# Kernel optimization log

Measured on AMD Instinct MI355X. Metric: run time of the kernel, lower is better.

Reference implementation:

```python
import jax, jax.numpy as jnp
import numpy as np

LN_EPS = 1e-5
GATE_EPS = 1e-9
TOP_K = 2
CAP_FACTOR = 1.0


def reference(x, gamma, beta, wg, W1, b1, W2, b2):
    B, S, H = x.shape
    E = wg.shape[1]
    T = B * S
    K = TOP_K
    C = int(np.ceil(K * T / E * CAP_FACTOR))  # per-expert capacity

    xf = x.reshape(T, H)
    # LayerNorm
    mu = jnp.mean(xf, axis=-1, keepdims=True)
    var = jnp.mean(jnp.square(xf - mu), axis=-1, keepdims=True)
    xn = (xf - mu) * jax.lax.rsqrt(var + LN_EPS) * gamma + beta

    # Gating (DeepSpeed top-k gate, softmax over experts)
    logits = xn @ wg                       # [T,E]
    gates = jax.nn.softmax(logits, axis=-1)
    vals, idx = jax.lax.top_k(gates, K)    # [T,K]

    # Capacity-aware positions: slot j priorities come after slots <j counts
    counts = jnp.zeros((E,), jnp.int32)
    pos_l, keep_l = [], []
    for j in range(K):
        oh = jax.nn.one_hot(idx[:, j], E, dtype=jnp.int32)  # [T,E]
        loc = jnp.cumsum(oh, axis=0) - 1 + counts[None, :]
        pos = jnp.sum(loc * oh, axis=1)                      # [T]
        counts = counts + jnp.sum(oh, axis=0)
        pos_l.append(pos)
        keep_l.append(pos < C)
    pos_k = jnp.stack(pos_l, axis=1)                         # [T,K]
    keep_k = jnp.stack(keep_l, axis=1)                       # [T,K]

    # Normalize kept gate values (DeepSpeed normalizes after capacity drop)
    kept = vals * keep_k.astype(vals.dtype)
    w = kept / (jnp.sum(kept, axis=1, keepdims=True) + GATE_EPS)  # [T,K]

    # Load-balancing aux loss (top-1 assignment counts, DeepSpeed style)
    me = jnp.mean(gates, axis=0)
    ce = jnp.mean(jax.nn.one_hot(idx[:, 0], E, dtype=gates.dtype), axis=0)
    l_aux = jnp.mean(me * ce) * E * E

    # Dispatch: scatter tokens into [E, C+1, H]; dropped tokens go to slot C (discarded)
    buf = jnp.zeros((E, C + 1, H), xn.dtype)
    pos_pad = jnp.where(keep_k, pos_k, C)                    # [T,K]
    for j in range(K):
        buf = buf.at[idx[:, j], pos_pad[:, j]].add(xn)

    # Grouped expert MLP
    h1 = jax.nn.gelu(jnp.einsum('ech,ehf->ecf', buf, W1) + b1[:, None, :], approximate=False)
    y = jnp.einsum('ecf,efh->ech', h1, W2) + b2[:, None, :]   # [E,C+1,H]

    # Combine: gather each token's expert outputs, weight, sum
    outf = jnp.zeros((T, H), x.dtype)
    for j in range(K):
        outf = outf + w[:, j, None] * y[idx[:, j], pos_pad[:, j]]

    out = x + outf.reshape(B, S, H)
    return out, l_aux, counts.astype(jnp.float32)


def setup_inputs() -> dict:
    key = jax.random.key(0)
    ks = jax.random.split(key, 6)
    H, E, F = 1024, 8, 4096
    x = jax.random.normal(ks[0], (2, 2048, H), jnp.float32)
    return {
        'x': x,
        'gamma': jnp.ones((H,), jnp.float32),
        'beta': jnp.zeros((H,), jnp.float32),
        'wg': jax.random.normal(ks[1], (H, E), jnp.float32) * 0.02,
        'W1': jax.random.normal(ks[2], (E, H, F), jnp.float32) * 0.02,
        'b1': jnp.zeros((E, F), jnp.float32),
        'W2': jax.random.normal(ks[3], (E, F, H), jnp.float32) * 0.02,
        'b2': jnp.zeros((E, H), jnp.float32),
    }
```

## Files before the change

kernel.cpp:

```cpp
#include <hip/hip_runtime.h>
#include <hip/hip_bf16.h>
#include <math.h>


#define T_TOK 4096
#define HD 1024
#define NE 8
#define FD 4096
#define CAPN 1024

typedef __attribute__((ext_vector_type(8))) short short8;
typedef __attribute__((ext_vector_type(4))) float f32x4;

__device__ __forceinline__ unsigned short f2b(float f) {
  __hip_bfloat16 h = __float2bfloat16(f);
  unsigned short u;
  __builtin_memcpy(&u, &h, 2);
  return u;
}

__global__ __launch_bounds__(256) void k_ln_gate(
    const float* __restrict__ x, const float* __restrict__ gamma,
    const float* __restrict__ beta, const float* __restrict__ wg,
    unsigned short* __restrict__ xn, float* __restrict__ gates,
    float2* __restrict__ vals, int2* __restrict__ eidx) {
  const int t = blockIdx.x;
  const int tid = threadIdx.x;
  const int lane = tid & 63, wid = tid >> 6;
  __shared__ float red[4];
  __shared__ float pr[4][8];

  const float4 v = ((const float4*)(x + (size_t)t * HD))[tid];
  float s = v.x + v.y + v.z + v.w;
#pragma unroll
  for (int o = 32; o > 0; o >>= 1) s += __shfl_down(s, o);
  if (lane == 0) red[wid] = s;
  __syncthreads();
  const float mean = (red[0] + red[1] + red[2] + red[3]) * (1.0f / HD);
  float dv[4];
  dv[0] = v.x - mean; dv[1] = v.y - mean; dv[2] = v.z - mean; dv[3] = v.w - mean;
  float q = dv[0]*dv[0] + dv[1]*dv[1] + dv[2]*dv[2] + dv[3]*dv[3];
  __syncthreads();
#pragma unroll
  for (int o = 32; o > 0; o >>= 1) q += __shfl_down(q, o);
  if (lane == 0) red[wid] = q;
  __syncthreads();
  const float var = (red[0] + red[1] + red[2] + red[3]) * (1.0f / HD);
  const float rs = 1.0f / sqrtf(var + 1e-5f);

  const float4 gm = ((const float4*)gamma)[tid];
  const float4 bt = ((const float4*)beta)[tid];
  float xv[4];
  xv[0] = dv[0] * rs * gm.x + bt.x;
  xv[1] = dv[1] * rs * gm.y + bt.y;
  xv[2] = dv[2] * rs * gm.z + bt.z;
  xv[3] = dv[3] * rs * gm.w + bt.w;
  ushort4 o4;
  o4.x = f2b(xv[0]); o4.y = f2b(xv[1]); o4.z = f2b(xv[2]); o4.w = f2b(xv[3]);
  ((ushort4*)(xn + (size_t)t * HD))[tid] = o4;

  float p[8];
#pragma unroll
  for (int e = 0; e < 8; e++) p[e] = 0.f;
  const int c0 = tid * 4;
#pragma unroll
  for (int i = 0; i < 4; i++) {
    const float4 w0 = ((const float4*)(wg + (size_t)(c0 + i) * NE))[0];
    const float4 w1 = ((const float4*)(wg + (size_t)(c0 + i) * NE))[1];
    p[0] += xv[i] * w0.x; p[1] += xv[i] * w0.y;
    p[2] += xv[i] * w0.z; p[3] += xv[i] * w0.w;
    p[4] += xv[i] * w1.x; p[5] += xv[i] * w1.y;
    p[6] += xv[i] * w1.z; p[7] += xv[i] * w1.w;
  }
#pragma unroll
  for (int e = 0; e < 8; e++)
#pragma unroll
    for (int o = 32; o > 0; o >>= 1) p[e] += __shfl_down(p[e], o);
  if (lane == 0) {
#pragma unroll
    for (int e = 0; e < 8; e++) pr[wid][e] = p[e];
  }
  __syncthreads();
  if (tid == 0) {
    float lg[8];
#pragma unroll
    for (int e = 0; e < 8; e++) lg[e] = pr[0][e] + pr[1][e] + pr[2][e] + pr[3][e];
    float mx = lg[0];
#pragma unroll
    for (int e = 1; e < 8; e++) mx = fmaxf(mx, lg[e]);
    float ex[8], sum = 0.f;
#pragma unroll
    for (int e = 0; e < 8; e++) { ex[e] = expf(lg[e] - mx); sum += ex[e]; }
    const float inv = 1.0f / sum;
    float g[8];
#pragma unroll
    for (int e = 0; e < 8; e++) { g[e] = ex[e] * inv; gates[(size_t)t * 8 + e] = g[e]; }
    int i0 = 0;
    for (int e = 1; e < 8; e++) if (g[e] > g[i0]) i0 = e;
    int i1 = (i0 == 0) ? 1 : 0;
    for (int e = 0; e < 8; e++) if (e != i0 && g[e] > g[i1]) i1 = e;
    vals[t] = make_float2(g[i0], g[i1]);
    eidx[t] = make_int2(i0, i1);
  }
}

__global__ __launch_bounds__(64) void k_scan(
    const int2* __restrict__ eidx, const float2* __restrict__ vals,
    const float* __restrict__ gates, int* __restrict__ ppad,
    float2* __restrict__ w, float* __restrict__ out_tail) {
  __shared__ int s0[T_TOK], s1[T_TOK];
  const int lane = threadIdx.x;
  for (int i = lane; i < T_TOK; i += 64) {
    int2 e2 = eidx[i];
    s0[i] = e2.x; s1[i] = e2.y;
  }
  __syncthreads();
  const unsigned long long lt = (lane == 63) ? 0x7fffffffffffffffull
                                             : ((1ull << lane) - 1ull);
  int cnt[8], ce[8];
#pragma unroll
  for (int e = 0; e < 8; e++) cnt[e] = 0;
  for (int j = 0; j < 2; j++) {
    const int* sj = j ? s1 : s0;
    for (int base = 0; base < T_TOK; base += 64) {
      const int my = sj[base + lane];
      int pos = 0;
#pragma unroll
      for (int e = 0; e < 8; e++) {
        unsigned long long m = __ballot(my == e);
        if (my == e) pos = cnt[e] + __popcll(m & lt);
        cnt[e] += __popcll(m);
      }
      ppad[(base + lane) * 2 + j] = (pos < CAPN) ? pos : CAPN;
    }
    if (j == 0) {
#pragma unroll
      for (int e = 0; e < 8; e++) ce[e] = cnt[e];
    }
  }
  for (int base = 0; base < T_TOK; base += 64) {
    const int t = base + lane;
    const float2 v = vals[t];
    const int p0 = ppad[2 * t], p1 = ppad[2 * t + 1];
    const float k0 = (p0 < CAPN) ? v.x : 0.f;
    const float k1 = (p1 < CAPN) ? v.y : 0.f;
    const float inv = 1.0f / (k0 + k1 + 1e-9f);
    w[t] = make_float2(k0 * inv, k1 * inv);
  }
  float acc[8];
#pragma unroll
  for (int e = 0; e < 8; e++) acc[e] = 0.f;
  for (int t = lane; t < T_TOK; t += 64) {
    const float4 a = ((const float4*)(gates + (size_t)t * 8))[0];
    const float4 b = ((const float4*)(gates + (size_t)t * 8))[1];
    acc[0] += a.x; acc[1] += a.y; acc[2] += a.z; acc[3] += a.w;
    acc[4] += b.x; acc[5] += b.y; acc[6] += b.z; acc[7] += b.w;
  }
#pragma unroll
  for (int e = 0; e < 8; e++)
#pragma unroll
    for (int o = 32; o > 0; o >>= 1) acc[e] += __shfl_down(acc[e], o);
  if (lane == 0) {
    float la = 0.f;
#pragma unroll
    for (int e = 0; e < 8; e++)
      la += (acc[e] * (1.0f / T_TOK)) * ((float)ce[e] * (1.0f / T_TOK));
    out_tail[0] = la * 8.0f;
#pragma unroll
    for (int e = 0; e < 8; e++) out_tail[1 + e] = (float)cnt[e];
  }
}

__global__ __launch_bounds__(128) void k_scatter(
    const unsigned short* __restrict__ xn, const int2* __restrict__ eidx,
    const int* __restrict__ ppad, unsigned short* __restrict__ buf) {
  const int b = blockIdx.x;
  const int t = b >> 1, j = b & 1;
  const int pp = ppad[2 * t + j];
  if (pp >= CAPN) return;
  const int2 e2 = eidx[t];
  const int e = j ? e2.y : e2.x;
  const uint4* s = (const uint4*)(xn + (size_t)t * HD);
  uint4* d = (uint4*)(buf + ((size_t)e * CAPN + pp) * HD);
  d[threadIdx.x] = s[threadIdx.x];
}

__global__ __launch_bounds__(256) void k_convT(
    const float* __restrict__ Win, unsigned short* __restrict__ Wout,
    int R, int C) {
  __shared__ __align__(16) unsigned short tile[64][72];
  const int e = blockIdx.z;
  const int c0 = blockIdx.x * 64, r0 = blockIdx.y * 64;
  const int tid = threadIdx.x;
  const int r = tid >> 2, qq = tid & 3;
  const float* src = Win + ((size_t)e * R + r0 + r) * C + c0;
#pragma unroll
  for (int i = 0; i < 4; i++) {
    const int cc = qq * 16 + i * 4;
    const float4 v = *(const float4*)(src + cc);
    tile[cc + 0][r] = f2b(v.x);
    tile[cc + 1][r] = f2b(v.y);
    tile[cc + 2][r] = f2b(v.z);
    tile[cc + 3][r] = f2b(v.w);
  }
  __syncthreads();
  const int cr = tid >> 2;
  unsigned short* dst = Wout + ((size_t)e * C + c0 + cr) * R + r0 + qq * 16;
  *(uint4*)(dst + 0) = *(const uint4*)&tile[cr][qq * 16];
  *(uint4*)(dst + 8) = *(const uint4*)&tile[cr][qq * 16 + 8];
}

template <int MODE>
__global__ __launch_bounds__(256) void k_gemm(
    const unsigned short* __restrict__ A, const unsigned short* __restrict__ Bt,
    const float* __restrict__ bias, void* __restrict__ out) {
  constexpr int K = MODE ? FD : HD;
  constexpr int N = MODE ? HD : FD;
  const int nt = blockIdx.x, mt = blockIdx.y;
  const int e = mt >> 3;
  const size_t m0 = (size_t)mt * 128;
  const int n0 = nt * 128;
  __shared__ __align__(16) unsigned short lA[128 * 32];
  __shared__ __align__(16) unsigned short lB[128 * 32];
  const int tid = threadIdx.x;
  const int lane = tid & 63, wid = tid >> 6;
  const int sr = tid >> 2, sq = tid & 3;
  const unsigned short* gA = A + m0 * (size_t)K + (size_t)sq * 8;
  const unsigned short* gB = Bt + ((size_t)e * N + n0) * K + (size_t)sq * 8;
  const int wr = wid >> 1, wc = wid & 1;
  const int l15 = lane & 15, half = lane >> 4;

  f32x4 acc[4][4];
  const f32x4 fz = {0.f, 0.f, 0.f, 0.f};
#pragma unroll
  for (int mi = 0; mi < 4; mi++)
#pragma unroll
    for (int ni = 0; ni < 4; ni++) acc[mi][ni] = fz;

  for (int k0 = 0; k0 < K; k0 += 32) {
    __syncthreads();
    __builtin_amdgcn_global_load_lds(
        (const __attribute__((address_space(1))) void*)(gA + (size_t)sr * K + k0),
        (__attribute__((address_space(3))) void*)(lA + wid * 512), 16, 0, 0);
    __builtin_amdgcn_global_load_lds(
        (const __attribute__((address_space(1))) void*)(gA + (size_t)(sr + 64) * K + k0),
        (__attribute__((address_space(3))) void*)(lA + 2048 + wid * 512), 16, 0, 0);
    __builtin_amdgcn_global_load_lds(
        (const __attribute__((address_space(1))) void*)(gB + (size_t)sr * K + k0),
        (__attribute__((address_space(3))) void*)(lB + wid * 512), 16, 0, 0);
    __builtin_amdgcn_global_load_lds(
        (const __attribute__((address_space(1))) void*)(gB + (size_t)(sr + 64) * K + k0),
        (__attribute__((address_space(3))) void*)(lB + 2048 + wid * 512), 16, 0, 0);
    __syncthreads();
    short8 af[4], bfr[4];
#pragma unroll
    for (int i = 0; i < 4; i++) {
      af[i]  = *(const short8*)&lA[(wr * 64 + i * 16 + l15) * 32 + half * 8];
      bfr[i] = *(const short8*)&lB[(wc * 64 + i * 16 + l15) * 32 + half * 8];
    }
#pragma unroll
    for (int mi = 0; mi < 4; mi++)
#pragma unroll
      for (int ni = 0; ni < 4; ni++)
        acc[mi][ni] = __builtin_amdgcn_mfma_f32_16x16x32_bf16(af[mi], bfr[ni],
                                                              acc[mi][ni], 0, 0, 0);
  }

  const float* brow = bias + (size_t)e * N;
  if (MODE == 0) {
    unsigned short* h1 = (unsigned short*)out;
#pragma unroll
    for (int mi = 0; mi < 4; mi++)
#pragma unroll
      for (int ni = 0; ni < 4; ni++) {
        const int col = n0 + wc * 64 + ni * 16 + l15;
        const float bv = brow[col];
#pragma unroll
        for (int r = 0; r < 4; r++) {
          const size_t row = m0 + wr * 64 + mi * 16 + half * 4 + r;
          const float pre = acc[mi][ni][r] + bv;
          const float g = 0.5f * pre * (1.0f + erff(pre * 0.70710678118654752f));
          h1[row * (size_t)N + col] = f2b(g);
        }
      }
  } else {
    float* y = (float*)out;
#pragma unroll
    for (int mi = 0; mi < 4; mi++)
#pragma unroll
      for (int ni = 0; ni < 4; ni++) {
        const int col = n0 + wc * 64 + ni * 16 + l15;
        const float bv = brow[col];
#pragma unroll
        for (int r = 0; r < 4; r++) {
          const size_t row = m0 + wr * 64 + mi * 16 + half * 4 + r;
          y[row * (size_t)N + col] = acc[mi][ni][r] + bv;
        }
      }
  }
}

__global__ __launch_bounds__(256) void k_combine(
    const float* __restrict__ x, const float* __restrict__ y,
    const int2* __restrict__ eidx, const int* __restrict__ ppad,
    const float2* __restrict__ w, float* __restrict__ out) {
  const int t = blockIdx.x, tid = threadIdx.x;
  const float2 wt = w[t];
  const int2 e2 = eidx[t];
  const int p0 = ppad[2 * t], p1 = ppad[2 * t + 1];
  float4 o = ((const float4*)(x + (size_t)t * HD))[tid];
  if (p0 < CAPN) {
    const float4 a = ((const float4*)(y + ((size_t)e2.x * CAPN + p0) * HD))[tid];
    o.x += wt.x * a.x; o.y += wt.x * a.y; o.z += wt.x * a.z; o.w += wt.x * a.w;
  }
  if (p1 < CAPN) {
    const float4 a = ((const float4*)(y + ((size_t)e2.y * CAPN + p1) * HD))[tid];
    o.x += wt.y * a.x; o.y += wt.y * a.y; o.z += wt.y * a.z; o.w += wt.y * a.w;
  }
  ((float4*)(out + (size_t)t * HD))[tid] = o;
}

extern "C" void kernel_launch(void* const* d_in, const int* in_sizes, int n_in,
                              void* d_out, int out_size, void* d_ws, size_t ws_size,
                              hipStream_t stream) {
  const float* x     = (const float*)d_in[0];
  const float* gamma = (const float*)d_in[1];
  const float* beta  = (const float*)d_in[2];
  const float* wg    = (const float*)d_in[3];
  const float* W1    = (const float*)d_in[4];
  const float* b1    = (const float*)d_in[5];
  const float* W2    = (const float*)d_in[6];
  const float* b2    = (const float*)d_in[7];
  float* out = (float*)d_out;

  char* ws = (char*)d_ws;
  unsigned short* xn  = (unsigned short*)(ws);
  unsigned short* buf = (unsigned short*)(ws + (8ull << 20));
  unsigned short* h1  = (unsigned short*)(ws + (24ull << 20));
  float* y            = (float*)(ws + (88ull << 20));
  unsigned short* WT  = (unsigned short*)(ws + (120ull << 20));
  float* gates        = (float*)(ws + (184ull << 20));
  float2* vals        = (float2*)(ws + (184ull << 20) + (128ull << 10));
  int2* eidx          = (int2*)(ws + (184ull << 20) + (160ull << 10));
  int* ppad           = (int*)(ws + (184ull << 20) + (192ull << 10));
  float2* wnrm        = (float2*)(ws + (184ull << 20) + (224ull << 10));

  hipMemsetAsync(buf, 0, (16ull << 20), stream);
  k_ln_gate<<<T_TOK, 256, 0, stream>>>(x, gamma, beta, wg, xn, gates, vals, eidx);
  k_scan<<<1, 64, 0, stream>>>(eidx, vals, gates, ppad, wnrm,
                               out + (size_t)T_TOK * HD);
  k_scatter<<<T_TOK * 2, 128, 0, stream>>>(xn, eidx, ppad, buf);
  k_convT<<<dim3(FD / 64, HD / 64, NE), 256, 0, stream>>>(W1, WT, HD, FD);
  k_gemm<0><<<dim3(FD / 128, 64), 256, 0, stream>>>(buf, WT, b1, h1);
  k_convT<<<dim3(HD / 64, FD / 64, NE), 256, 0, stream>>>(W2, WT, FD, HD);
  k_gemm<1><<<dim3(HD / 128, 64), 256, 0, stream>>>(h1, WT, b2, y);
  k_combine<<<T_TOK, 256, 0, stream>>>(x, y, eidx, ppad, wnrm, out);
}
```

Measured before the change: 633.1 us.

## Use 256x256 pipelined MFMA GEMM with split-K down-projection and fused combine

Replaces the 128x128 single-buffered expert GEMM with a 512-thread, 256x256-tile kernel. It uses a 4-stage LDS ring fed by global_load_lds, XOR-swizzled LDS addressing, explicit waitcnt/barrier scheduling, setprio around the MFMA bursts and a grouped block-index swizzle. The down-projection can split K in two into separate partial buffers, and the combine kernel sums them, adds b2 and computes the capacity-normalized gate weights inline. The buffer memset is dropped and the scan kernel runs the gate-mean reduction on extra waves. The aim is more data reuse per tile and better overlap of loads with MFMA, at the cost of 128KB of LDS per block (one block per CU) and extra fp32 partial-output traffic in the split-K path.

```diff
diff --git a/kernel.cpp b/kernel.cpp
--- a/kernel.cpp
+++ b/kernel.cpp
@@ -104,70 +104,77 @@
   }
 }
 
-__global__ __launch_bounds__(64) void k_scan(
-    const int2* __restrict__ eidx, const float2* __restrict__ vals,
-    const float* __restrict__ gates, int* __restrict__ ppad,
-    float2* __restrict__ w, float* __restrict__ out_tail) {
+__global__ __launch_bounds__(256) void k_scan(
+    const int2* __restrict__ eidx, const float* __restrict__ gates,
+    int* __restrict__ ppad, float* __restrict__ out_tail) {
   __shared__ int s0[T_TOK], s1[T_TOK];
-  const int lane = threadIdx.x;
-  for (int i = lane; i < T_TOK; i += 64) {
+  __shared__ float mw[3][8];
+  __shared__ int ce_sh[8], cnt_sh[8];
+  const int tid = threadIdx.x;
+  const int lane = tid & 63, wid = tid >> 6;
+  for (int i = tid; i < T_TOK; i += 256) {
     int2 e2 = eidx[i];
     s0[i] = e2.x; s1[i] = e2.y;
   }
   __syncthreads();
-  const unsigned long long lt = (lane == 63) ? 0x7fffffffffffffffull
-                                             : ((1ull << lane) - 1ull);
-  int cnt[8], ce[8];
-#pragma unroll
-  for (int e = 0; e < 8; e++) cnt[e] = 0;
-  for (int j = 0; j < 2; j++) {
-    const int* sj = j ? s1 : s0;
-    for (int base = 0; base < T_TOK; base += 64) {
-      const int my = sj[base + lane];
-      int pos = 0;
-#pragma unroll
-      for (int e = 0; e < 8; e++) {
-        unsigned long long m = __ballot(my == e);
-        if (my == e) pos = cnt[e] + __popcll(m & lt);
-        cnt[e] += __popcll(m);
+  if (wid == 0) {
+    const unsigned long long lt = (lane == 63) ? 0x7fffffffffffffffull
+                                               : ((1ull << lane) - 1ull);
+    int cnt[8];
+#pragma unroll
+    for (int e = 0; e < 8; e++) cnt[e] = 0;
+    for (int j = 0; j < 2; j++) {
+      const int* sj = j ? s1 : s0;
+      for (int base = 0; base < T_TOK; base += 64) {
+        const int my = sj[base + lane];
+        int pos = 0;
+#pragma unroll
+        for (int e = 0; e < 8; e++) {
+          unsigned long long m = __ballot(my == e);
+          if (my == e) pos = cnt[e] + __popcll(m & lt);
+          cnt[e] += __popcll(m);
+        }
+        ppad[(base + lane) * 2 + j] = (pos < CAPN) ? pos : CAPN;
       }
-      ppad[(base + lane) * 2 + j] = (pos < CAPN) ? pos : CAPN;
-    }
-    if (j == 0) {
-#pragma unroll
-      for (int e = 0; e < 8; e++) ce[e] = cnt[e];
-    }
-  }
-  for (int base = 0; base < T_TOK; base += 64) {
-    const int t = base + lane;
-    const float2 v = vals[t];
-    const int p0 = ppad[2 * t], p1 = ppad[2 * t + 1];
-    const float k0 = (p0 < CAPN) ? v.x : 0.f;
-    const float k1 = (p1 < CAPN) ? v.y : 0.f;
-    const float inv = 1.0f / (k0 + k1 + 1e-9f);
-    w[t] = make_float2(k0 * inv, k1 * inv);
-  }
-  float acc[8];
-#pragma unroll
-  for (int e = 0; e < 8; e++) acc[e] = 0.f;
-  for (int t = lane; t < T_TOK; t += 64) {
-    const float4 a = ((const float4*)(gates + (size_t)t * 8))[0];
-    const float4 b = ((const float4*)(gates + (size_t)t * 8))[1];
-    acc[0] += a.x; acc[1] += a.y; acc[2] += a.z; acc[3] += a.w;
-    acc[4] += b.x; acc[5] += b.y; acc[6] += b.z; acc[7] += b.w;
-  }
-#pragma unroll
-  for (int e = 0; e < 8; e++)
-#pragma unroll
-    for (int o = 32; o > 0; o >>= 1) acc[e] += __shfl_down(acc[e], o);
-  if (lane == 0) {
+      if (j == 0 && lane == 0) {
+#pragma unroll
+        for (int e = 0; e < 8; e++) ce_sh[e] = cnt[e];
+      }
+    }
+    if (lane == 0) {
+#pragma unroll
+      for (int e = 0; e < 8; e++) cnt_sh[e] = cnt[e];
+    }
+  } else {
+    float acc[8];
+#pragma unroll
+    for (int e = 0; e < 8; e++) acc[e] = 0.f;
+    for (int t = tid - 64; t < T_TOK; t += 192) {
+      const float4 a = ((const float4*)(gates + (size_t)t * 8))[0];
+      const float4 b = ((const float4*)(gates + (size_t)t * 8))[1];
+      acc[0] += a.x; acc[1] += a.y; acc[2] += a.z; acc[3] += a.w;
+      acc[4] += b.x; acc[5] += b.y; acc[6] += b.z; acc[7] += b.w;
+    }
+#pragma unroll
+    for (int e = 0; e < 8; e++)
+#pragma unroll
+      for (int o = 32; o > 0; o >>= 1) acc[e] += __shfl_down(acc[e], o);
+    if (lane == 0) {
+#pragma unroll
+      for (int e = 0; e < 8; e++) mw[wid - 1][e] = acc[e];
+    }
+  }
+  __syncthreads();
+  if (tid == 0) {
     float la = 0.f;
 #pragma unroll
-    for (int e = 0; e < 8; e++)
-      la += (acc[e] * (1.0f / T_TOK)) * ((float)ce[e] * (1.0f / T_TOK));
+    for (int e = 0; e < 8; e++) {
+      const float me = (mw[0][e] + mw[1][e] + mw[2][e]) * (1.0f / T_TOK);
+      la += me * ((float)ce_sh[e] * (1.0f / T_TOK));
+    }
     out_tail[0] = la * 8.0f;
 #pragma unroll
-    for (int e = 0; e < 8; e++) out_tail[1 + e] = (float)cnt[e];
+    for (int e = 0; e < 8; e++) out_tail[1 + e] = (float)cnt_sh[e];
   }
 }
 
@@ -210,112 +217,180 @@
   *(uint4*)(dst + 8) = *(const uint4*)&tile[cr][qq * 16 + 8];
 }
 
-template <int MODE>
-__global__ __launch_bounds__(256) void k_gemm(
+#define GLL16(SRC, DSTOFF) __builtin_amdgcn_global_load_lds( \
+    (const __attribute__((address_space(1))) void*)(SRC), \
+    (__attribute__((address_space(3))) void*)(smem + (DSTOFF)), 16, 0, 0)
+
+#define STAGE_A(T) { const size_t ko = (size_t)(T) * 32; const int rbo = ((T)&3)*32768; \
+  GLL16(gA + ko + oA0, rbo + ldsAd); \
+  GLL16(gA + ko + oA1, rbo + 8192 + ldsAd); }
+
+#define STAGE_B(T) { const size_t ko = (size_t)(T) * 32; const int rbo = ((T)&3)*32768; \
+  GLL16(gB + ko + oA0, rbo + ldsBd); \
+  GLL16(gB + ko + oA1, rbo + 8192 + ldsBd); }
+
+#define TILE(T, DOST, VMW) { \
+  const unsigned char* rb = smem + ((T)&3)*32768; \
+  short8 af[4], bfv[4]; \
+  _Pragma("unroll") for (int i = 0; i < 4; ++i) { \
+    af[i]  = *(const short8*)(rb + offA + i*1024); \
+    bfv[i] = *(const short8*)(rb + offB + i*1024); } \
+  if (DOST) { STAGE_A((T)+3); } \
+  asm volatile("s_barrier" ::: "memory"); \
+  __builtin_amdgcn_s_setprio(1); \
+  _Pragma("unroll") for (int mi = 0; mi < 4; ++mi) \
+    _Pragma("unroll") for (int ni = 0; ni < 4; ++ni) \
+      acc[mi][ni] = __builtin_amdgcn_mfma_f32_16x16x32_bf16(af[mi], bfv[ni], acc[mi][ni], 0, 0, 0); \
+  __builtin_amdgcn_s_setprio(0); \
+  _Pragma("unroll") for (int i = 0; i < 4; ++i) \
+    af[i] = *(const short8*)(rb + offA + 4096 + i*1024); \
+  if (DOST) { STAGE_B((T)+3); } \
+  asm volatile("s_waitcnt lgkmcnt(0)" ::: "memory"); \
+  asm volatile("s_waitcnt vmcnt(" #VMW ")" ::: "memory"); \
+  asm volatile("s_barrier" ::: "memory"); \
+  __builtin_amdgcn_s_setprio(1); \
+  _Pragma("unroll") for (int mi = 0; mi < 4; ++mi) \
+    _Pragma("unroll") for (int ni = 0; ni < 4; ++ni) \
+      acc[4+mi][ni] = __builtin_amdgcn_mfma_f32_16x16x32_bf16(af[mi], bfv[ni], acc[4+mi][ni], 0, 0, 0); \
+  __builtin_amdgcn_s_setprio(0); \
+}
+
+template <int MODE, int SPLITK>
+__global__ __launch_bounds__(512, 2) void k_gemm256(
     const unsigned short* __restrict__ A, const unsigned short* __restrict__ Bt,
     const float* __restrict__ bias, void* __restrict__ out) {
   constexpr int K = MODE ? FD : HD;
   constexpr int N = MODE ? HD : FD;
-  const int nt = blockIdx.x, mt = blockIdx.y;
-  const int e = mt >> 3;
-  const size_t m0 = (size_t)mt * 128;
-  const int n0 = nt * 128;
-  __shared__ __align__(16) unsigned short lA[128 * 32];
-  __shared__ __align__(16) unsigned short lB[128 * 32];
+  constexpr int KLOC = K / SPLITK;
+  constexpr int NT = KLOC / 32;
+  constexpr int NBT = N / 256;
+
+  __shared__ __align__(16) unsigned char smem[4 * 32768];
+
   const int tid = threadIdx.x;
   const int lane = tid & 63, wid = tid >> 6;
-  const int sr = tid >> 2, sq = tid & 3;
-  const unsigned short* gA = A + m0 * (size_t)K + (size_t)sq * 8;
-  const unsigned short* gB = Bt + ((size_t)e * N + n0) * K + (size_t)sq * 8;
-  const int wr = wid >> 1, wc = wid & 1;
-  const int l15 = lane & 15, half = lane >> 4;
-
-  f32x4 acc[4][4];
+  const int l15 = lane & 15, lq = lane >> 4;
+  const int wr = wid >> 2, wc = wid & 3;
+
+  const int nwg = gridDim.x;
+  const int per = nwg >> 3;
+  const int lin = blockIdx.x;
+  const int swz = (lin & 7) * per + (lin >> 3);
+  const int mt = swz & 31;
+  const int rest = swz >> 5;
+  const int nt = rest % NBT;
+  const int z = rest / NBT;
+
+  const int e = mt >> 2;
+  const size_t m0 = (size_t)mt * 256;
+  const int n0 = nt * 256;
+  const unsigned short* gA = A + m0 * (size_t)K + (size_t)z * KLOC;
+  const unsigned short* gB = Bt + ((size_t)e * N + n0) * (size_t)K + (size_t)z * KLOC;
+
+  const int LA0 = tid * 16, LA1 = 8192 + tid * 16;
+  const int r0s = LA0 >> 6, c0s = (LA0 >> 4) & 3;
+  const int r1s = LA1 >> 6, c1s = (LA1 >> 4) & 3;
+  const size_t oA0 = (size_t)r0s * K + (size_t)(c0s ^ ((r0s >> 1) & 3)) * 8;
+  const size_t oA1 = (size_t)r1s * K + (size_t)(c1s ^ ((r1s >> 1) & 3)) * 8;
+  const int ldsAd = wid * 1024;
+  const int ldsBd = 16384 + wid * 1024;
+
+  const int rA = wr * 128 + l15;
+  const int offA = rA * 64 + ((lq ^ ((rA >> 1) & 3)) << 4);
+  const int rB = wc * 64 + l15;
+  const int offB = 16384 + rB * 64 + ((lq ^ ((rB >> 1) & 3)) << 4);
+
+  f32x4 acc[8][4];
   const f32x4 fz = {0.f, 0.f, 0.f, 0.f};
 #pragma unroll
-  for (int mi = 0; mi < 4; mi++)
+  for (int mi = 0; mi < 8; mi++)
 #pragma unroll
     for (int ni = 0; ni < 4; ni++) acc[mi][ni] = fz;
 
-  for (int k0 = 0; k0 < K; k0 += 32) {
-    __syncthreads();
-    __builtin_amdgcn_global_load_lds(
-        (const __attribute__((address_space(1))) void*)(gA + (size_t)sr * K + k0),
-        (__attribute__((address_space(3))) void*)(lA + wid * 512), 16, 0, 0);
-    __builtin_amdgcn_global_load_lds(
-        (const __attribute__((address_space(1))) void*)(gA + (size_t)(sr + 64) * K + k0),
-        (__attribute__((address_space(3))) void*)(lA + 2048 + wid * 512), 16, 0, 0);
-    __builtin_amdgcn_global_load_lds(
-        (const __attribute__((address_space(1))) void*)(gB + (size_t)sr * K + k0),
-        (__attribute__((address_space(3))) void*)(lB + wid * 512), 16, 0, 0);
-    __builtin_amdgcn_global_load_lds(
-        (const __attribute__((address_space(1))) void*)(gB + (size_t)(sr + 64) * K + k0),
-        (__attribute__((address_space(3))) void*)(lB + 2048 + wid * 512), 16, 0, 0);
-    __syncthreads();
-    short8 af[4], bfr[4];
-#pragma unroll
-    for (int i = 0; i < 4; i++) {
-      af[i]  = *(const short8*)&lA[(wr * 64 + i * 16 + l15) * 32 + half * 8];
-      bfr[i] = *(const short8*)&lB[(wc * 64 + i * 16 + l15) * 32 + half * 8];
-    }
-#pragma unroll
-    for (int mi = 0; mi < 4; mi++)
-#pragma unroll
-      for (int ni = 0; ni < 4; ni++)
-        acc[mi][ni] = __builtin_amdgcn_mfma_f32_16x16x32_bf16(af[mi], bfr[ni],
-                                                              acc[mi][ni], 0, 0, 0);
-  }
-
-  const float* brow = bias + (size_t)e * N;
+  STAGE_A(0); STAGE_B(0);
+  STAGE_A(1); STAGE_B(1);
+  STAGE_A(2); STAGE_B(2);
+  asm volatile("s_waitcnt vmcnt(8)" ::: "memory");
+  asm volatile("s_barrier" ::: "memory");
+
+  for (int t = 0; t <= NT - 4; ++t) { TILE(t, true, 8); }
+  TILE(NT - 3, false, 4);
+  TILE(NT - 2, false, 0);
+  TILE(NT - 1, false, 63);
+
   if (MODE == 0) {
-    unsigned short* h1 = (unsigned short*)out;
-#pragma unroll
-    for (int mi = 0; mi < 4; mi++)
-#pragma unroll
-      for (int ni = 0; ni < 4; ni++) {
+    unsigned short* o = (unsigned short*)out;
+    const float* brow = bias + (size_t)e * N;
+#pragma unroll
+    for (int mi = 0; mi < 8; ++mi)
+#pragma unroll
+      for (int ni = 0; ni < 4; ++ni) {
         const int col = n0 + wc * 64 + ni * 16 + l15;
         const float bv = brow[col];
 #pragma unroll
-        for (int r = 0; r < 4; r++) {
-          const size_t row = m0 + wr * 64 + mi * 16 + half * 4 + r;
+        for (int r = 0; r < 4; ++r) {
+          const size_t row = m0 + wr * 128 + mi * 16 + lq * 4 + r;
           const float pre = acc[mi][ni][r] + bv;
           const float g = 0.5f * pre * (1.0f + erff(pre * 0.70710678118654752f));
-          h1[row * (size_t)N + col] = f2b(g);
+          o[row * (size_t)N + col] = f2b(g);
         }
       }
   } else {
-    float* y = (float*)out;
-#pragma unroll
-    for (int mi = 0; mi < 4; mi++)
-#pragma unroll
-      for (int ni = 0; ni < 4; ni++) {
+    float* yp = (float*)out + (size_t)z * (8192ull * 1024ull);
+#pragma unroll
+    for (int mi = 0; mi < 8; ++mi)
+#pragma unroll
+      for (int ni = 0; ni < 4; ++ni) {
         const int col = n0 + wc * 64 + ni * 16 + l15;
-        const float bv = brow[col];
-#pragma unroll
-        for (int r = 0; r < 4; r++) {
-          const size_t row = m0 + wr * 64 + mi * 16 + half * 4 + r;
-          y[row * (size_t)N + col] = acc[mi][ni][r] + bv;
+#pragma unroll
+        for (int r = 0; r < 4; ++r) {
+          const size_t row = m0 + wr * 128 + mi * 16 + lq * 4 + r;
+          yp[row * (size_t)N + col] = acc[mi][ni][r];
         }
       }
   }
 }
-
+#undef TILE
+#undef STAGE_A
+#undef STAGE_B
+#undef GLL16
+
+template <int SPLIT>
 __global__ __launch_bounds__(256) void k_combine(
-    const float* __restrict__ x, const float* __restrict__ y,
+    const float* __restrict__ x, const float* __restrict__ y0,
+    const float* __restrict__ y1, const float* __restrict__ b2,
     const int2* __restrict__ eidx, const int* __restrict__ ppad,
-    const float2* __restrict__ w, float* __restrict__ out) {
+    const float2* __restrict__ vals, float* __restrict__ out) {
   const int t = blockIdx.x, tid = threadIdx.x;
-  const float2 wt = w[t];
+  const float2 v = vals[t];
   const int2 e2 = eidx[t];
   const int p0 = ppad[2 * t], p1 = ppad[2 * t + 1];
+  const float k0 = (p0 < CAPN) ? v.x : 0.f;
+  const float k1 = (p1 < CAPN) ? v.y : 0.f;
+  const float inv = 1.0f / (k0 + k1 + 1e-9f);
+  const float w0 = k0 * inv, w1 = k1 * inv;
   float4 o = ((const float4*)(x + (size_t)t * HD))[tid];
   if (p0 < CAPN) {
-    const float4 a = ((const float4*)(y + ((size_t)e2.x * CAPN + p0) * HD))[tid];
-    o.x += wt.x * a.x; o.y += wt.x * a.y; o.z += wt.x * a.z; o.w += wt.x * a.w;
+    const size_t s = ((size_t)e2.x * CAPN + p0) * HD;
+    float4 a = ((const float4*)(y0 + s))[tid];
+    if (SPLIT == 2) {
+      const float4 b = ((const float4*)(y1 + s))[tid];
+      a.x += b.x; a.y += b.y; a.z += b.z; a.w += b.w;
+    }
+    const float4 bb = ((const float4*)(b2 + (size_t)e2.x * HD))[tid];
+    o.x += w0 * (a.x + bb.x); o.y += w0 * (a.y + bb.y);
+    o.z += w0 * (a.z + bb.z); o.w += w0 * (a.w + bb.w);
   }
   if (p1 < CAPN) {
-    const float4 a = ((const float4*)(y + ((size_t)e2.y * CAPN + p1) * HD))[tid];
-    o.x += wt.y * a.x; o.y += wt.y * a.y; o.z += wt.y * a.z; o.w += wt.y * a.w;
+    const size_t s = ((size_t)e2.y * CAPN + p1) * HD;
+    float4 a = ((const float4*)(y0 + s))[tid];
+    if (SPLIT == 2) {
+      const float4 b = ((const float4*)(y1 + s))[tid];
+      a.x += b.x; a.y += b.y; a.z += b.z; a.w += b.w;
+    }
+    const float4 bb = ((const float4*)(b2 + (size_t)e2.y * HD))[tid];
+    o.x += w1 * (a.x + bb.x); o.y += w1 * (a.y + bb.y);
+    o.z += w1 * (a.z + bb.z); o.w += w1 * (a.w + bb.w);
   }
   ((float4*)(out + (size_t)t * HD))[tid] = o;
 }
@@ -334,25 +409,29 @@
   float* out = (float*)d_out;
 
   char* ws = (char*)d_ws;
-  unsigned short* xn  = (unsigned short*)(ws);
-  unsigned short* buf = (unsigned short*)(ws + (8ull << 20));
-  unsigned short* h1  = (unsigned short*)(ws + (24ull << 20));
-  float* y            = (float*)(ws + (88ull << 20));
-  unsigned short* WT  = (unsigned short*)(ws + (120ull << 20));
-  float* gates        = (float*)(ws + (184ull << 20));
-  float2* vals        = (float2*)(ws + (184ull << 20) + (128ull << 10));
-  int2* eidx          = (int2*)(ws + (184ull << 20) + (160ull << 10));
-  int* ppad           = (int*)(ws + (184ull << 20) + (192ull << 10));
-  float2* wnrm        = (float2*)(ws + (184ull << 20) + (224ull << 10));
-
-  hipMemsetAsync(buf, 0, (16ull << 20), stream);
+  float* gates        = (float*)(ws);
+  float2* vals        = (float2*)(ws + (128ull << 10));
+  int2* eidx          = (int2*)(ws + (160ull << 10));
+  int* ppad           = (int*)(ws + (192ull << 10));
+  unsigned short* xn  = (unsigned short*)(ws + (512ull << 10));
+  unsigned short* buf = (unsigned short*)(ws + (512ull << 10) + (8ull << 20));
+  unsigned short* h1  = (unsigned short*)(ws + (512ull << 10) + (24ull << 20));
+  unsigned short* WT  = (unsigned short*)(ws + (512ull << 10) + (88ull << 20));
+  float* y0           = (float*)(ws + (512ull << 10) + (152ull << 20));
+  float* y1           = (float*)(ws + (512ull << 10) + (184ull << 20));
+  const bool splitk = ws_size >= ((217ull << 20));
+
   k_ln_gate<<<T_TOK, 256, 0, stream>>>(x, gamma, beta, wg, xn, gates, vals, eidx);
-  k_scan<<<1, 64, 0, stream>>>(eidx, vals, gates, ppad, wnrm,
-                               out + (size_t)T_TOK * HD);
+  k_scan<<<1, 256, 0, stream>>>(eidx, gates, ppad, out + (size_t)T_TOK * HD);
   k_scatter<<<T_TOK * 2, 128, 0, stream>>>(xn, eidx, ppad, buf);
   k_convT<<<dim3(FD / 64, HD / 64, NE), 256, 0, stream>>>(W1, WT, HD, FD);
-  k_gemm<0><<<dim3(FD / 128, 64), 256, 0, stream>>>(buf, WT, b1, h1);
+  k_gemm256<0, 1><<<512, 512, 0, stream>>>(buf, WT, b1, h1);
   k_convT<<<dim3(HD / 64, FD / 64, NE), 256, 0, stream>>>(W2, WT, FD, HD);
-  k_gemm<1><<<dim3(HD / 128, 64), 256, 0, stream>>>(h1, WT, b2, y);
-  k_combine<<<T_TOK, 256, 0, stream>>>(x, y, eidx, ppad, wnrm, out);
-}
+  if (splitk) {
+    k_gemm256<1, 2><<<256, 512, 0, stream>>>(h1, WT, nullptr, y0);
+    k_combine<2><<<T_TOK, 256, 0, stream>>>(x, y0, y1, b2, eidx, ppad, vals, out);
+  } else {
+    k_gemm256<1, 1><<<128, 512, 0, stream>>>(h1, WT, nullptr, y0);
+    k_combine<1><<<T_TOK, 256, 0, stream>>>(x, y0, y1, b2, eidx, ppad, vals, out);
+  }
+}
```

Result: faster. 556.4 us (-12.1%).
